# Performance work log

Measured on AMD Instinct MI355X. Metric: run time of the kernel, lower is better.

## Reference

```python
import jax, jax.numpy as jnp
import numpy as np

B, T, N, D, H, L = 8, 200, 512, 4, 64, 32


def setup_inputs() -> dict:
    key = jax.random.key(0)
    ks = jax.random.split(key, 7)
    s = 1.0 / np.sqrt(H)  # torch GRU/Linear default init scale
    x = jax.random.normal(ks[0], (B, T, N, D), dtype=jnp.float32)
    W_ih = jax.random.uniform(ks[1], (3 * H, D), minval=-s, maxval=s, dtype=jnp.float32)
    W_hh = jax.random.uniform(ks[2], (3 * H, H), minval=-s, maxval=s, dtype=jnp.float32)
    b_ih = jax.random.uniform(ks[3], (3 * H,), minval=-s, maxval=s, dtype=jnp.float32)
    b_hh = jax.random.uniform(ks[4], (3 * H,), minval=-s, maxval=s, dtype=jnp.float32)
    W_enc = jax.random.uniform(ks[5], (L, H), minval=-s, maxval=s, dtype=jnp.float32)
    b_enc = jax.random.uniform(ks[6], (L,), minval=-s, maxval=s, dtype=jnp.float32)
    return {"trajectories": x, "W_ih": W_ih, "W_hh": W_hh, "b_ih": b_ih,
            "b_hh": b_hh, "W_enc": W_enc, "b_enc": b_enc}


def _gru_last_hidden(x, W_ih, W_hh, b_ih, b_hh):
    # x: [M, T, D] -> last hidden [M, H]; PyTorch GRU gate order (r, z, n)
    gx = jnp.einsum('mtd,gd->mtg', x, W_ih) + b_ih  # [M, T, 3H], input gates precomputed

    def step(h, gxt):
        gh = h @ W_hh.T + b_hh                      # [M, 3H]
        rz = jax.nn.sigmoid(gxt[:, :2 * H] + gh[:, :2 * H])
        r, z = rz[:, :H], rz[:, H:]
        n = jnp.tanh(gxt[:, 2 * H:] + r * gh[:, 2 * H:])
        h = (1.0 - z) * n + z * h
        return h, None

    h0 = jnp.zeros((x.shape[0], H), dtype=x.dtype)
    hT, _ = jax.lax.scan(step, h0, jnp.swapaxes(gx, 0, 1))  # scan over T
    return hT


def reference(trajectories, W_ih, W_hh, b_ih, b_hh, W_enc, b_enc):
    b, t, n, d = trajectories.shape
    # permute(1,0,2) per clip == move object axis before time, flatten all trajectories
    x = jnp.transpose(trajectories, (0, 2, 1, 3)).reshape(b * n, t, d)  # [M, T, D]
    hT = _gru_last_hidden(x, W_ih, W_hh, b_ih, b_hh)                    # [M, H]
    out = hT @ W_enc.T + b_enc                                          # [M, L]
    return out.reshape(b, n, L)  # list of [N, L] per clip, stacked
```

## Files before the change

### kernel.cpp

```cpp
#include <hip/hip_runtime.h>

#define TT 200
#define NN 512
#define DD 4
#define HH 64
#define LL 32
#define SB 16
#define BPB (NN / SB)
#define KP 72
#define LOG2E 1.44269504088896340736f

typedef short bf16x8 __attribute__((ext_vector_type(8)));
typedef float f32x4 __attribute__((ext_vector_type(4)));

union U8 { unsigned short s[8]; unsigned u[4]; bf16x8 v; };

__device__ __forceinline__ void split2(float x, unsigned short& hi, unsigned short& lo) {
    unsigned u = __float_as_uint(x);
    hi = (unsigned short)(u >> 16);
    float lf = x - __uint_as_float(u & 0xffff0000u);
    lo = (unsigned short)(__float_as_uint(lf) >> 16);
}

__global__ __launch_bounds__(512, 1)
void gru_traj_kernel(const float* __restrict__ xg,
                     const float* __restrict__ W_ih,
                     const float* __restrict__ W_hh,
                     const float* __restrict__ b_ih,
                     const float* __restrict__ b_hh,
                     const float* __restrict__ W_enc,
                     const float* __restrict__ b_enc,
                     float* __restrict__ out)
{
    __shared__ __align__(16) unsigned short hhi[2][SB][KP];
    __shared__ __align__(16) unsigned short hlo[2][SB][KP];
    __shared__ __align__(16) float hsf[SB][HH + 4];

    const int tid = threadIdx.x;
    const int bid = blockIdx.x;
    const int b   = bid >> 5;
    const int n0  = (bid & (BPB - 1)) * SB;

    const int w  = tid >> 6;
    const int wq = w & 3;
    const int wg = w >> 2;
    const int l  = tid & 63;
    const int lr = l & 15;
    const int lg = l >> 4;
    const int u0 = 16 * wq + lg * 4;
    const int ub = u0 + 2 * wg;

    const float sc[3] = { LOG2E, LOG2E, 2.0f * LOG2E };

    bf16x8 awh[3][2];
    #pragma unroll
    for (int i = 0; i < 3; ++i) {
        const int g = i * 64 + 16 * wq + lr;
        #pragma unroll
        for (int kc = 0; kc < 2; ++kc) {
            const float* p = W_hh + g * HH + kc * 32 + lg * 8;
            U8 uh;
            #pragma unroll
            for (int j = 0; j < 8; ++j) {
                unsigned short hi, lo;
                split2(p[j] * sc[i], hi, lo);
                uh.s[j] = hi; (void)lo;
            }
            awh[i][kc] = uh.v;
        }
    }
    float wihc[3][2][4], cbrz[2][2], cbx[2], cbh[2];
    #pragma unroll
    for (int i = 0; i < 3; ++i) {
        #pragma unroll
        for (int k = 0; k < 2; ++k) {
            const int g = i * 64 + ub + k;
            #pragma unroll
            for (int d = 0; d < 4; ++d) wihc[i][k][d] = W_ih[g * DD + d] * sc[i];
            if (i < 2) cbrz[i][k] = (b_ih[g] + b_hh[g]) * sc[i];
            else       { cbx[k] = b_ih[g] * sc[2]; cbh[k] = b_hh[g] * sc[2]; }
        }
    }

    for (int idx = tid; idx < 2 * SB * KP / 2; idx += 512) {
        reinterpret_cast<unsigned*>(hhi)[idx] = 0u;
        reinterpret_cast<unsigned*>(hlo)[idx] = 0u;
    }
    float hreg[2] = {0.f, 0.f};

    float4 xc = *reinterpret_cast<const float4*>(
        xg + ((size_t)(b * TT) * NN + n0 + lr) * DD);
    __syncthreads();

    const bool hihalf = (wg != 0);
    const f32x4 z4 = {0.f, 0.f, 0.f, 0.f};

    #pragma unroll 2
    for (int t = 0; t < TT; ++t) {
        const int cur = t & 1, nxt = cur ^ 1;
        const int tn  = (t + 1 < TT) ? t + 1 : t;

        float4 xn = *reinterpret_cast<const float4*>(
            xg + ((size_t)(b * TT + tn) * NN + n0 + lr) * DD);

        bf16x8 bh0 = *reinterpret_cast<const bf16x8*>(&hhi[cur][lr][lg * 8]);
        bf16x8 bh1 = *reinterpret_cast<const bf16x8*>(&hhi[cur][lr][32 + lg * 8]);
        bf16x8 bl0 = *reinterpret_cast<const bf16x8*>(&hlo[cur][lr][lg * 8]);
        bf16x8 bl1 = *reinterpret_cast<const bf16x8*>(&hlo[cur][lr][32 + lg * 8]);

        float gxv[3][2];
        #pragma unroll
        for (int i = 0; i < 3; ++i) {
            #pragma unroll
            for (int k = 0; k < 2; ++k) {
                const float c0 = (i < 2) ? cbrz[i][k] : cbx[k];
                gxv[i][k] = fmaf(wihc[i][k][0], xc.x, fmaf(wihc[i][k][1], xc.y,
                            fmaf(wihc[i][k][2], xc.z, fmaf(wihc[i][k][3], xc.w, c0))));
            }
        }

        f32x4 aR = __builtin_amdgcn_mfma_f32_16x16x32_bf16(awh[0][0], bl0, z4, 0,0,0);
        f32x4 aZ = __builtin_amdgcn_mfma_f32_16x16x32_bf16(awh[1][0], bl0, z4, 0,0,0);
        f32x4 aN = __builtin_amdgcn_mfma_f32_16x16x32_bf16(awh[2][0], bl0, z4, 0,0,0);
        aR = __builtin_amdgcn_mfma_f32_16x16x32_bf16(awh[0][1], bl1, aR, 0,0,0);
        aZ = __builtin_amdgcn_mfma_f32_16x16x32_bf16(awh[1][1], bl1, aZ, 0,0,0);
        aN = __builtin_amdgcn_mfma_f32_16x16x32_bf16(awh[2][1], bl1, aN, 0,0,0);
        aR = __builtin_amdgcn_mfma_f32_16x16x32_bf16(awh[0][0], bh0, aR, 0,0,0);
        aZ = __builtin_amdgcn_mfma_f32_16x16x32_bf16(awh[1][0], bh0, aZ, 0,0,0);
        aN = __builtin_amdgcn_mfma_f32_16x16x32_bf16(awh[2][0], bh0, aN, 0,0,0);
        aR = __builtin_amdgcn_mfma_f32_16x16x32_bf16(awh[0][1], bh1, aR, 0,0,0);
        aZ = __builtin_amdgcn_mfma_f32_16x16x32_bf16(awh[1][1], bh1, aZ, 0,0,0);
        aN = __builtin_amdgcn_mfma_f32_16x16x32_bf16(awh[2][1], bh1, aN, 0,0,0);

        float vR0 = hihalf ? aR[2] : aR[0];
        float vR1 = hihalf ? aR[3] : aR[1];
        float vZ0 = hihalf ? aZ[2] : aZ[0];
        float vZ1 = hihalf ? aZ[3] : aZ[1];
        float vN0 = hihalf ? aN[2] : aN[0];
        float vN1 = hihalf ? aN[3] : aN[1];

        float hn0, hn1;
        {
            float sR  = vR0 + gxv[0][0];
            float sZ  = vZ0 + gxv[1][0];
            float ghn = vN0 + cbh[0];
            float rg = __builtin_amdgcn_rcpf(1.0f + __builtin_amdgcn_exp2f(-sR));
            float ez = __builtin_amdgcn_exp2f(-sZ);
            float na = fmaf(rg, ghn, gxv[2][0]);
            float e  = __builtin_amdgcn_exp2f(-na);
            float nn = fmaf(2.0f, __builtin_amdgcn_rcpf(1.0f + e), -1.0f);
            float z  = __builtin_amdgcn_rcpf(1.0f + ez);
            hn0 = fmaf(z, hreg[0] - nn, nn);
            hreg[0] = hn0;
        }
        {
            float sR  = vR1 + gxv[0][1];
            float sZ  = vZ1 + gxv[1][1];
            float ghn = vN1 + cbh[1];
            float rg = __builtin_amdgcn_rcpf(1.0f + __builtin_amdgcn_exp2f(-sR));
            float ez = __builtin_amdgcn_exp2f(-sZ);
            float na = fmaf(rg, ghn, gxv[2][1]);
            float e  = __builtin_amdgcn_exp2f(-na);
            float nn = fmaf(2.0f, __builtin_amdgcn_rcpf(1.0f + e), -1.0f);
            float z  = __builtin_amdgcn_rcpf(1.0f + ez);
            hn1 = fmaf(z, hreg[1] - nn, nn);
            hreg[1] = hn1;
        }

        unsigned ph = __builtin_amdgcn_perm(__float_as_uint(hn1), __float_as_uint(hn0),
                                            0x07060302u);
        float lf0 = hn0 - __uint_as_float(__float_as_uint(hn0) & 0xffff0000u);
        float lf1 = hn1 - __uint_as_float(__float_as_uint(hn1) & 0xffff0000u);
        unsigned pl = __builtin_amdgcn_perm(__float_as_uint(lf1), __float_as_uint(lf0),
                                            0x07060302u);
        *reinterpret_cast<unsigned*>(&hhi[nxt][lr][ub]) = ph;
        *reinterpret_cast<unsigned*>(&hlo[nxt][lr][ub]) = pl;
        xc = xn;
        __syncthreads();
    }

    hsf[lr][ub]     = hreg[0];
    hsf[lr][ub + 1] = hreg[1];
    __syncthreads();
    {
        const int s = tid >> 5, li = tid & 31;
        float a = b_enc[li];
        #pragma unroll
        for (int k = 0; k < HH; ++k)
            a = fmaf(hsf[s][k], W_enc[li * HH + k], a);
        out[(bid * SB + s) * LL + li] = a;
    }
}

extern "C" void kernel_launch(void* const* d_in, const int* in_sizes, int n_in,
                              void* d_out, int out_size, void* d_ws, size_t ws_size,
                              hipStream_t stream) {
    const float* xg    = (const float*)d_in[0];
    const float* W_ih  = (const float*)d_in[1];
    const float* W_hh  = (const float*)d_in[2];
    const float* b_ih  = (const float*)d_in[3];
    const float* b_hh  = (const float*)d_in[4];
    const float* W_enc = (const float*)d_in[5];
    const float* b_enc = (const float*)d_in[6];
    float* out = (float*)d_out;

    dim3 grid(8 * BPB), block(512);
    hipLaunchKernelGGL(gru_traj_kernel, grid, block, 0, stream,
                       xg, W_ih, W_hh, b_ih, b_hh, W_enc, b_enc, out);
}
```

Before: 105.1 us.

## Halve sequences per block to run two 4-wave blocks per CU

Each block now handles 8 trajectories with 256 threads instead of 16 with 512. Sequences are mapped onto duplicated MFMA columns instead of duplicated wave groups, and two blocks are allowed per CU. The aim is to shrink the per-step barrier to 4 waves and let two independent recurrent chains interleave to hide latency. In exchange, half of each MFMA's columns are redundant, so total matrix work stays about the same.

```diff
diff --git a/kernel.cpp b/kernel.cpp
--- a/kernel.cpp
+++ b/kernel.cpp
@@ -5,7 +5,7 @@
 #define DD 4
 #define HH 64
 #define LL 32
-#define SB 16
+#define SB 8
 #define BPB (NN / SB)
 #define KP 72
 #define LOG2E 1.44269504088896340736f
@@ -22,7 +22,7 @@
     lo = (unsigned short)(__float_as_uint(lf) >> 16);
 }
 
-__global__ __launch_bounds__(512, 1)
+__global__ __launch_bounds__(256, 2)
 void gru_traj_kernel(const float* __restrict__ xg,
                      const float* __restrict__ W_ih,
                      const float* __restrict__ W_hh,
@@ -38,33 +38,33 @@
 
     const int tid = threadIdx.x;
     const int bid = blockIdx.x;
-    const int b   = bid >> 5;
+    const int b   = bid >> 6;
     const int n0  = (bid & (BPB - 1)) * SB;
 
     const int w  = tid >> 6;
-    const int wq = w & 3;
-    const int wg = w >> 2;
     const int l  = tid & 63;
     const int lr = l & 15;
     const int lg = l >> 4;
-    const int u0 = 16 * wq + lg * 4;
-    const int ub = u0 + 2 * wg;
+    const int s  = l & 7;
+    const int hi8 = (lr >> 3) & 1;
+    const int u0 = 16 * w + lg * 4;
+    const int ub = u0 + 2 * hi8;
 
     const float sc[3] = { LOG2E, LOG2E, 2.0f * LOG2E };
 
     bf16x8 awh[3][2];
     #pragma unroll
     for (int i = 0; i < 3; ++i) {
-        const int g = i * 64 + 16 * wq + lr;
+        const int g = i * 64 + 16 * w + lr;
         #pragma unroll
         for (int kc = 0; kc < 2; ++kc) {
             const float* p = W_hh + g * HH + kc * 32 + lg * 8;
             U8 uh;
             #pragma unroll
             for (int j = 0; j < 8; ++j) {
-                unsigned short hi, lo;
-                split2(p[j] * sc[i], hi, lo);
-                uh.s[j] = hi; (void)lo;
+                unsigned short hh, ll_;
+                split2(p[j] * sc[i], hh, ll_);
+                uh.s[j] = hh; (void)ll_;
             }
             awh[i][kc] = uh.v;
         }
@@ -82,17 +82,17 @@
         }
     }
 
-    for (int idx = tid; idx < 2 * SB * KP / 2; idx += 512) {
+    for (int idx = tid; idx < 2 * SB * KP / 2; idx += 256) {
         reinterpret_cast<unsigned*>(hhi)[idx] = 0u;
         reinterpret_cast<unsigned*>(hlo)[idx] = 0u;
     }
     float hreg[2] = {0.f, 0.f};
 
     float4 xc = *reinterpret_cast<const float4*>(
-        xg + ((size_t)(b * TT) * NN + n0 + lr) * DD);
+        xg + ((size_t)(b * TT) * NN + n0 + s) * DD);
     __syncthreads();
 
-    const bool hihalf = (wg != 0);
+    const bool hi8b = (hi8 != 0);
     const f32x4 z4 = {0.f, 0.f, 0.f, 0.f};
 
     #pragma unroll 2
@@ -101,12 +101,12 @@
         const int tn  = (t + 1 < TT) ? t + 1 : t;
 
         float4 xn = *reinterpret_cast<const float4*>(
-            xg + ((size_t)(b * TT + tn) * NN + n0 + lr) * DD);
-
-        bf16x8 bh0 = *reinterpret_cast<const bf16x8*>(&hhi[cur][lr][lg * 8]);
-        bf16x8 bh1 = *reinterpret_cast<const bf16x8*>(&hhi[cur][lr][32 + lg * 8]);
-        bf16x8 bl0 = *reinterpret_cast<const bf16x8*>(&hlo[cur][lr][lg * 8]);
-        bf16x8 bl1 = *reinterpret_cast<const bf16x8*>(&hlo[cur][lr][32 + lg * 8]);
+            xg + ((size_t)(b * TT + tn) * NN + n0 + s) * DD);
+
+        bf16x8 bh0 = *reinterpret_cast<const bf16x8*>(&hhi[cur][s][lg * 8]);
+        bf16x8 bh1 = *reinterpret_cast<const bf16x8*>(&hhi[cur][s][32 + lg * 8]);
+        bf16x8 bl0 = *reinterpret_cast<const bf16x8*>(&hlo[cur][s][lg * 8]);
+        bf16x8 bl1 = *reinterpret_cast<const bf16x8*>(&hlo[cur][s][32 + lg * 8]);
 
         float gxv[3][2];
         #pragma unroll
@@ -132,12 +132,12 @@
         aZ = __builtin_amdgcn_mfma_f32_16x16x32_bf16(awh[1][1], bh1, aZ, 0,0,0);
         aN = __builtin_amdgcn_mfma_f32_16x16x32_bf16(awh[2][1], bh1, aN, 0,0,0);
 
-        float vR0 = hihalf ? aR[2] : aR[0];
-        float vR1 = hihalf ? aR[3] : aR[1];
-        float vZ0 = hihalf ? aZ[2] : aZ[0];
-        float vZ1 = hihalf ? aZ[3] : aZ[1];
-        float vN0 = hihalf ? aN[2] : aN[0];
-        float vN1 = hihalf ? aN[3] : aN[1];
+        float vR0 = hi8b ? aR[2] : aR[0];
+        float vR1 = hi8b ? aR[3] : aR[1];
+        float vZ0 = hi8b ? aZ[2] : aZ[0];
+        float vZ1 = hi8b ? aZ[3] : aZ[1];
+        float vN0 = hi8b ? aN[2] : aN[0];
+        float vN1 = hi8b ? aN[3] : aN[1];
 
         float hn0, hn1;
         {
@@ -173,22 +173,22 @@
         float lf1 = hn1 - __uint_as_float(__float_as_uint(hn1) & 0xffff0000u);
         unsigned pl = __builtin_amdgcn_perm(__float_as_uint(lf1), __float_as_uint(lf0),
                                             0x07060302u);
-        *reinterpret_cast<unsigned*>(&hhi[nxt][lr][ub]) = ph;
-        *reinterpret_cast<unsigned*>(&hlo[nxt][lr][ub]) = pl;
+        *reinterpret_cast<unsigned*>(&hhi[nxt][s][ub]) = ph;
+        *reinterpret_cast<unsigned*>(&hlo[nxt][s][ub]) = pl;
         xc = xn;
         __syncthreads();
     }
 
-    hsf[lr][ub]     = hreg[0];
-    hsf[lr][ub + 1] = hreg[1];
+    hsf[s][ub]     = hreg[0];
+    hsf[s][ub + 1] = hreg[1];
     __syncthreads();
     {
-        const int s = tid >> 5, li = tid & 31;
+        const int so = tid >> 5, li = tid & 31;
         float a = b_enc[li];
         #pragma unroll
         for (int k = 0; k < HH; ++k)
-            a = fmaf(hsf[s][k], W_enc[li * HH + k], a);
-        out[(bid * SB + s) * LL + li] = a;
+            a = fmaf(hsf[so][k], W_enc[li * HH + k], a);
+        out[(bid * SB + so) * LL + li] = a;
     }
 }
 
@@ -204,7 +204,7 @@
     const float* b_enc = (const float*)d_in[6];
     float* out = (float*)d_out;
 
-    dim3 grid(8 * BPB), block(512);
+    dim3 grid(8 * BPB), block(256);
     hipLaunchKernelGGL(gru_traj_kernel, grid, block, 0, stream,
                        xg, W_ih, W_hh, b_ih, b_hh, W_enc, b_enc, out);
 }
```

After: 101.8 us. -3.1%, faster.
